# Performance work log

Hardware: AMD Instinct MI355X
Metric: run time of the kernel (lower is better)

## Reference

```python
import jax, jax.numpy as jnp
import numpy as np

N, E, D, G = 20000, 640000, 256, 64
BN_EPS = 1e-5


def setup_inputs() -> dict:
    key = jax.random.key(0)
    ks = jax.random.split(key, 16)
    p = lambda k, sh: jax.random.normal(k, sh, dtype=jnp.float32) * 0.05
    x = jax.random.normal(ks[0], (N, D), dtype=jnp.float32)
    edge_index = jax.random.randint(ks[1], (2, E), 0, N, dtype=jnp.int32)
    batch = jnp.sort(jax.random.randint(ks[2], (N,), 0, G, dtype=jnp.int32))
    return dict(
        x=x, edge_index=edge_index, batch=batch,
        W1=p(ks[3], (D, D)), a1_src=p(ks[4], (D,)), a1_dst=p(ks[5], (D,)), b1=p(ks[6], (D,)),
        W2=p(ks[7], (D, D)), a2_src=p(ks[8], (D,)), a2_dst=p(ks[9], (D,)), b2=p(ks[10], (D,)),
        bn_gamma=jnp.ones((D,), jnp.float32), bn_beta=jnp.zeros((D,), jnp.float32),
        bn_mean=jnp.zeros((D,), jnp.float32), bn_var=jnp.ones((D,), jnp.float32),
        Wl=p(ks[11], (D, D)), bl=p(ks[12], (D,)),
    )


def gat_conv(x, src, dst, W, a_src, a_dst, b):
    # PyG GATConv, heads=1, concat=True, negative_slope=0.2, self-loops already appended
    h = x @ W                               # [N, D]
    alpha_s = h @ a_src                     # [N]
    alpha_d = h @ a_dst                     # [N]
    e = jax.nn.leaky_relu(alpha_s[src] + alpha_d[dst], 0.2)   # [E+N]
    # segment softmax over edges grouped by destination node
    m = jax.ops.segment_max(e, dst, num_segments=N)
    ex = jnp.exp(e - m[dst])
    s = jax.ops.segment_sum(ex, dst, num_segments=N)
    alpha = ex / s[dst]                     # self-loops guarantee s > 0
    out = jax.ops.segment_sum(alpha[:, None] * h[src], dst, num_segments=N)
    return out + b


def reference(x, edge_index, batch, W1, a1_src, a1_dst, b1, W2, a2_src, a2_dst, b2,
              bn_gamma, bn_beta, bn_mean, bn_var, Wl, bl):
    loop = jnp.arange(N, dtype=edge_index.dtype)
    src = jnp.concatenate([edge_index[0], loop])
    dst = jnp.concatenate([edge_index[1], loop])

    h = jax.nn.leaky_relu(gat_conv(x, src, dst, W1, a1_src, a1_dst, b1), 0.01)
    h = jax.nn.leaky_relu(gat_conv(h, src, dst, W2, a2_src, a2_dst, b2), 0.01)
    # BatchNorm over nodes (eval mode, running stats)
    h = (h - bn_mean) * jax.lax.rsqrt(bn_var + BN_EPS) * bn_gamma + bn_beta
    # global mean pool per graph, then linear (dropout is identity in eval)
    sums = jax.ops.segment_sum(h, batch, num_segments=G)           # [G, D]
    cnt = jax.ops.segment_sum(jnp.ones((N,), h.dtype), batch, num_segments=G)
    pooled = sums / jnp.maximum(cnt, 1.0)[:, None]
    return pooled @ Wl.T + bl
```

## Files before the change

### kernel.cpp

```cpp
#include <hip/hip_runtime.h>
#include <hip/hip_bf16.h>

#define NN 20000
#define EE 640000
#define DD 256
#define GG 64
#define ETOT (EE + NN)
#define BN_EPS 1e-5f

typedef short s16x8 __attribute__((ext_vector_type(8)));
typedef short s16x4 __attribute__((ext_vector_type(4)));
typedef float f32x4 __attribute__((ext_vector_type(4)));
typedef int   i32x2 __attribute__((ext_vector_type(2)));

__device__ __forceinline__ unsigned short f2bf_hi(float x) {
    unsigned u = __float_as_uint(x);
    unsigned r = (u + 0x7FFFu + ((u >> 16) & 1u)) >> 16;
    return (unsigned short)r;
}
__device__ __forceinline__ float bf2f(unsigned short h) {
    return __uint_as_float(((unsigned)h) << 16);
}

__global__ void prep_kernel(const int* __restrict__ batch, int* __restrict__ start,
                            float* __restrict__ cntf) {
    int g = threadIdx.x;
    if (g <= GG) {
        if (g == GG) start[GG] = NN;
        else {
            int lo = 0, hi = NN;
            while (lo < hi) { int mid = (lo + hi) >> 1; if (batch[mid] < g) lo = mid + 1; else hi = mid; }
            start[g] = lo;
        }
    }
    __syncthreads();
    if (g < GG) cntf[g] = (float)(start[g + 1] - start[g]);
}

__global__ void hist_kernel(const int* __restrict__ ei, int* __restrict__ counts) {
    int i = blockIdx.x * blockDim.x + threadIdx.x;
    int stride = gridDim.x * blockDim.x;
    for (; i < ETOT; i += stride) {
        int dst = (i < EE) ? ei[EE + i] : (i - EE);
        atomicAdd(&counts[dst], 1);
    }
}

#define SCHUNK 20
__global__ __launch_bounds__(1024) void scan_kernel(const int* __restrict__ counts,
                                                    int* __restrict__ offsets,
                                                    int* __restrict__ cursor) {
    __shared__ int wsums[16];
    int t = threadIdx.x, lane = t & 63, wid = t >> 6;
    int base = t * SCHUNK;
    int loc[SCHUNK];
    int sum = 0;
    #pragma unroll
    for (int i = 0; i < SCHUNK; ++i) {
        int idx = base + i;
        int v = (idx < NN) ? counts[idx] : 0;
        loc[i] = sum; sum += v;
    }
    int x = sum;
    #pragma unroll
    for (int o = 1; o < 64; o <<= 1) { int tv = __shfl_up(x, o, 64); if (lane >= o) x += tv; }
    if (lane == 63) wsums[wid] = x;
    __syncthreads();
    if (wid == 0) {
        int wv = (lane < 16) ? wsums[lane] : 0;
        #pragma unroll
        for (int o = 1; o < 16; o <<= 1) { int tv = __shfl_up(wv, o, 64); if (lane >= o) wv += tv; }
        if (lane < 16) wsums[lane] = wv;
    }
    __syncthreads();
    int tbase = (wid ? wsums[wid - 1] : 0) + x - sum;
    #pragma unroll
    for (int i = 0; i < SCHUNK; ++i) {
        int idx = base + i;
        if (idx < NN) { int e = tbase + loc[i]; offsets[idx] = e; cursor[idx] = e; }
    }
    if (t == 0) offsets[NN] = wsums[15];
}

__global__ void scatter_kernel(const int* __restrict__ ei, int* __restrict__ cursor,
                               int* __restrict__ csr_src) {
    int i = blockIdx.x * blockDim.x + threadIdx.x;
    int stride = gridDim.x * blockDim.x;
    for (; i < ETOT; i += stride) {
        int s, d;
        if (i < EE) { s = ei[i]; d = ei[EE + i]; }
        else        { s = i - EE; d = i - EE; }
        int pos = atomicAdd(&cursor[d], 1);
        csr_src[pos] = s;
    }
}

__global__ __launch_bounds__(256) void convB_kernel(const float* __restrict__ W1,
                                                    const float* __restrict__ W2,
                                                    short* __restrict__ BhT1,
                                                    short* __restrict__ BlT1,
                                                    short* __restrict__ BhT2,
                                                    short* __restrict__ BlT2) {
    int b = blockIdx.x;
    int n = b & 255, which = b >> 8;
    int k = threadIdx.x;
    const float* B = which ? W2 : W1;
    short* Bh = which ? BhT2 : BhT1;
    short* Bl = which ? BlT2 : BlT1;
    float x = B[k * DD + n];
    unsigned short hb = f2bf_hi(x);
    Bh[n * DD + k] = (short)hb;
    Bl[n * DD + k] = (short)f2bf_hi(x - bf2f(hb));
}

#define GBM 128
#define GBN 128
#define GBK 64

__global__ __launch_bounds__(256) void gemm_mfma_kernel(const float* __restrict__ A,
                                                        const short* __restrict__ BhT,
                                                        const short* __restrict__ BlT,
                                                        const float* __restrict__ a_src,
                                                        const float* __restrict__ a_dst,
                                                        short* __restrict__ hb,
                                                        float* __restrict__ asp,
                                                        float* __restrict__ adp,
                                                        int M) {
    __shared__ short As_h[GBM * GBK];
    __shared__ short As_l[GBM * GBK];
    __shared__ short Bs_h[GBN * GBK];
    __shared__ short Bs_l[GBN * GBK];
    int tid = threadIdx.x;
    int row0 = blockIdx.y * GBM;
    int col0 = blockIdx.x * GBN;
    int w = tid >> 6, lane = tid & 63;
    int wr = w >> 1, wc = w & 1;

    f32x4 acc[4][4];
    #pragma unroll
    for (int m = 0; m < 4; ++m)
        #pragma unroll
        for (int n = 0; n < 4; ++n)
            acc[m][n] = (f32x4){0.f, 0.f, 0.f, 0.f};

    int srow = tid >> 3;
    int sslot = tid & 7;

    for (int k0 = 0; k0 < DD; k0 += GBK) {
        __syncthreads();
        #pragma unroll
        for (int p = 0; p < 4; ++p) {
            int r = p * 32 + srow;
            int gr = row0 + r;
            float xv[8];
            if (gr < M) {
                const float4* ap = (const float4*)(A + (size_t)gr * DD + k0 + sslot * 8);
                float4 a0 = ap[0], a1 = ap[1];
                xv[0] = a0.x; xv[1] = a0.y; xv[2] = a0.z; xv[3] = a0.w;
                xv[4] = a1.x; xv[5] = a1.y; xv[6] = a1.z; xv[7] = a1.w;
            } else {
                #pragma unroll
                for (int i = 0; i < 8; ++i) xv[i] = 0.f;
            }
            s16x8 hv, lv;
            #pragma unroll
            for (int i = 0; i < 8; ++i) {
                unsigned short hbb = f2bf_hi(xv[i]);
                hv[i] = (short)hbb;
                lv[i] = (short)f2bf_hi(xv[i] - bf2f(hbb));
            }
            int byte = r * 128 + ((sslot ^ (r & 7)) << 4);
            *(s16x8*)((char*)As_h + byte) = hv;
            *(s16x8*)((char*)As_l + byte) = lv;
            const short* bhp = BhT + (size_t)(col0 + r) * DD + k0 + sslot * 8;
            const short* blp = BlT + (size_t)(col0 + r) * DD + k0 + sslot * 8;
            *(s16x8*)((char*)Bs_h + byte) = *(const s16x8*)bhp;
            *(s16x8*)((char*)Bs_l + byte) = *(const s16x8*)blp;
        }
        __syncthreads();

        #pragma unroll
        for (int ks = 0; ks < 2; ++ks) {
            s16x8 ah[4], al[4], bh[4], bl[4];
            int g = ks * 4 + (lane >> 4);
            #pragma unroll
            for (int m = 0; m < 4; ++m) {
                int r = wr * 64 + m * 16 + (lane & 15);
                int byte = r * 128 + ((g ^ (r & 7)) << 4);
                ah[m] = *(const s16x8*)((char*)As_h + byte);
                al[m] = *(const s16x8*)((char*)As_l + byte);
            }
            #pragma unroll
            for (int n = 0; n < 4; ++n) {
                int c = wc * 64 + n * 16 + (lane & 15);
                int byte = c * 128 + ((g ^ (c & 7)) << 4);
                bh[n] = *(const s16x8*)((char*)Bs_h + byte);
                bl[n] = *(const s16x8*)((char*)Bs_l + byte);
            }
            #pragma unroll
            for (int m = 0; m < 4; ++m)
                #pragma unroll
                for (int n = 0; n < 4; ++n) {
                    acc[m][n] = __builtin_amdgcn_mfma_f32_16x16x32_bf16(ah[m], bh[n], acc[m][n], 0, 0, 0);
                    acc[m][n] = __builtin_amdgcn_mfma_f32_16x16x32_bf16(ah[m], bl[n], acc[m][n], 0, 0, 0);
                    acc[m][n] = __builtin_amdgcn_mfma_f32_16x16x32_bf16(al[m], bh[n], acc[m][n], 0, 0, 0);
                }
        }
    }

    float vsrc[4], vdst[4];
    #pragma unroll
    for (int n = 0; n < 4; ++n) {
        int cg = col0 + wc * 64 + n * 16 + (lane & 15);
        vsrc[n] = a_src[cg];
        vdst[n] = a_dst[cg];
    }
    #pragma unroll
    for (int m = 0; m < 4; ++m) {
        #pragma unroll
        for (int j = 0; j < 4; ++j) {
            float ps = 0.f, pd = 0.f;
            #pragma unroll
            for (int n = 0; n < 4; ++n) {
                float c = acc[m][n][j];
                ps += c * vsrc[n];
                pd += c * vdst[n];
            }
            #pragma unroll
            for (int o = 1; o < 16; o <<= 1) {
                ps += __shfl_xor(ps, o, 64);
                pd += __shfl_xor(pd, o, 64);
            }
            if ((lane & 15) == 0) {
                int rg = row0 + wr * 64 + m * 16 + ((lane >> 4) << 2) + j;
                if (rg < M) {
                    asp[(size_t)(blockIdx.x * 2 + wc) * NN + rg] = ps;
                    adp[(size_t)(blockIdx.x * 2 + wc) * NN + rg] = pd;
                }
            }
        }
    }

    #pragma unroll
    for (int m = 0; m < 4; ++m) {
        int rbase = row0 + wr * 64 + m * 16 + ((lane >> 4) << 2);
        #pragma unroll
        for (int n = 0; n < 4; ++n) {
            int cg = col0 + wc * 64 + n * 16 + (lane & 15);
            #pragma unroll
            for (int j = 0; j < 4; ++j) {
                int rg = rbase + j;
                if (rg < M) hb[(size_t)rg * DD + cg] = (short)f2bf_hi(acc[m][n][j]);
            }
        }
    }
}

__global__ void reduce_kernel(const float* __restrict__ asp, const float* __restrict__ adp,
                              float* __restrict__ as_, float* __restrict__ ad_) {
    int i = blockIdx.x * blockDim.x + threadIdx.x;
    if (i < NN) {
        as_[i] = asp[i] + asp[NN + i] + asp[2 * NN + i] + asp[3 * NN + i];
        ad_[i] = adp[i] + adp[NN + i] + adp[2 * NN + i] + adp[3 * NN + i];
    }
}

__global__ __launch_bounds__(256) void alpha_kernel(const int* __restrict__ csr_src,
                                                    const int* __restrict__ offsets,
                                                    const float* __restrict__ as_,
                                                    const float* __restrict__ ad_,
                                                    int2* __restrict__ pairs) {
    int tid = threadIdx.x;
    int w = tid >> 6, lane = tid & 63;
    int node = blockIdx.x * 4 + w;
    int off = offsets[node];
    int deg = offsets[node + 1] - off;
    float adn = ad_[node];

    if (deg <= 64) {
        int si = 0; float e = -INFINITY;
        if (lane < deg) {
            si = csr_src[off + lane];
            float t = as_[si] + adn;
            e = (t > 0.f) ? t : 0.2f * t;
        }
        float m = e;
        #pragma unroll
        for (int o = 32; o > 0; o >>= 1) m = fmaxf(m, __shfl_xor(m, o, 64));
        float ex = (lane < deg) ? expf(e - m) : 0.f;
        float s = ex;
        #pragma unroll
        for (int o = 32; o > 0; o >>= 1) s += __shfl_xor(s, o, 64);
        if (lane < deg) {
            int2 p; p.x = si; p.y = __float_as_int(ex / s);
            pairs[off + lane] = p;
        }
        return;
    }

    float m = -INFINITY, s = 0.f;
    for (int cs = 0; cs < deg; cs += 64) {
        int cl = min(64, deg - cs);
        float e = -INFINITY;
        if (lane < cl) {
            int si = csr_src[off + cs + lane];
            float t = as_[si] + adn;
            e = (t > 0.f) ? t : 0.2f * t;
        }
        float cm = e;
        #pragma unroll
        for (int o = 32; o > 0; o >>= 1) cm = fmaxf(cm, __shfl_xor(cm, o, 64));
        float newm = fmaxf(m, cm);
        float ex = (lane < cl) ? expf(e - newm) : 0.f;
        float csum = ex;
        #pragma unroll
        for (int o = 32; o > 0; o >>= 1) csum += __shfl_xor(csum, o, 64);
        s = s * expf(m - newm) + csum;
        m = newm;
    }
    float inv = 1.f / s;
    for (int cs = 0; cs < deg; cs += 64) {
        int cl = min(64, deg - cs);
        if (lane < cl) {
            int si = csr_src[off + cs + lane];
            float t = as_[si] + adn;
            float e = (t > 0.f) ? t : 0.2f * t;
            int2 p; p.x = si; p.y = __float_as_int(expf(e - m) * inv);
            pairs[off + cs + lane] = p;
        }
    }
}

__global__ __launch_bounds__(256) void aggregate_kernel(const short* __restrict__ hb,
                                                        const int2* __restrict__ pairs,
                                                        const int* __restrict__ offsets,
                                                        const float* __restrict__ bias,
                                                        float* __restrict__ out) {
    int tid = threadIdx.x;
    int w = tid >> 6, lane = tid & 63;
    int b = blockIdx.x;
    int sl = b & 3;
    int node = ((b >> 2) << 2) + w;
    int eg = lane >> 3;
    int fl = lane & 7;
    int f0 = sl * 64 + fl * 8;
    int off = offsets[node];
    int deg = offsets[node + 1] - off;
    const i32x2* pp = (const i32x2*)pairs + off;

    float accA[8], accB[8];
    #pragma unroll
    for (int k = 0; k < 8; ++k) { accA[k] = 0.f; accB[k] = 0.f; }

    int j = 0;
    i32x2 qA, qB;
    if (deg >= 16) { qA = pp[eg]; qB = pp[8 + eg]; }
    for (; j + 32 <= deg; j += 16) {
        i32x2 nA = pp[j + 16 + eg];
        i32x2 nB = pp[j + 24 + eg];
        s16x8 hA = *(const s16x8*)(hb + (size_t)qA.x * DD + f0);
        s16x8 hB = *(const s16x8*)(hb + (size_t)qB.x * DD + f0);
        float aA = __int_as_float(qA.y), aB = __int_as_float(qB.y);
        #pragma unroll
        for (int k = 0; k < 8; ++k) accA[k] += aA * bf2f((unsigned short)hA[k]);
        #pragma unroll
        for (int k = 0; k < 8; ++k) accB[k] += aB * bf2f((unsigned short)hB[k]);
        qA = nA; qB = nB;
    }
    if (j + 16 <= deg) {
        s16x8 hA = *(const s16x8*)(hb + (size_t)qA.x * DD + f0);
        s16x8 hB = *(const s16x8*)(hb + (size_t)qB.x * DD + f0);
        float aA = __int_as_float(qA.y), aB = __int_as_float(qB.y);
        #pragma unroll
        for (int k = 0; k < 8; ++k) accA[k] += aA * bf2f((unsigned short)hA[k]);
        #pragma unroll
        for (int k = 0; k < 8; ++k) accB[k] += aB * bf2f((unsigned short)hB[k]);
        j += 16;
    }
    {
        if (j + eg < deg) {
            i32x2 p = pp[j + eg];
            s16x8 hv = *(const s16x8*)(hb + (size_t)p.x * DD + f0);
            float a = __int_as_float(p.y);
            #pragma unroll
            for (int k = 0; k < 8; ++k) accA[k] += a * bf2f((unsigned short)hv[k]);
        }
        if (j + 8 + eg < deg) {
            i32x2 p = pp[j + 8 + eg];
            s16x8 hv = *(const s16x8*)(hb + (size_t)p.x * DD + f0);
            float a = __int_as_float(p.y);
            #pragma unroll
            for (int k = 0; k < 8; ++k) accB[k] += a * bf2f((unsigned short)hv[k]);
        }
    }

    f32x4 r0, r1;
    #pragma unroll
    for (int k = 0; k < 8; ++k) {
        float v = accA[k] + accB[k];
        v += __shfl_xor(v, 8, 64);
        v += __shfl_xor(v, 16, 64);
        v += __shfl_xor(v, 32, 64);
        if (k < 4) r0[k] = v; else r1[k - 4] = v;
    }
    if (eg == 0) {
        const f32x4 b0 = *(const f32x4*)(bias + f0);
        const f32x4 b1 = *(const f32x4*)(bias + f0 + 4);
        #pragma unroll
        for (int k = 0; k < 4; ++k) {
            float v0 = r0[k] + b0[k];
            float v1 = r1[k] + b1[k];
            r0[k] = (v0 > 0.f) ? v0 : 0.01f * v0;
            r1[k] = (v1 > 0.f) ? v1 : 0.01f * v1;
        }
        __builtin_nontemporal_store(r0, (f32x4*)(out + (size_t)node * DD + f0));
        __builtin_nontemporal_store(r1, (f32x4*)(out + (size_t)node * DD + f0 + 4));
    }
}

#define PSLICE 8
__global__ __launch_bounds__(256) void pool_kernel(const float* __restrict__ h,
                                                   const int* __restrict__ start,
                                                   float* __restrict__ pool) {
    int g = blockIdx.x >> 3, sl = blockIdx.x & (PSLICE - 1);
    int f = threadIdx.x;
    int s0 = start[g], s1 = start[g + 1];
    float acc = 0.f;
    for (int nd = s0 + sl; nd < s1; nd += PSLICE)
        acc += h[(size_t)nd * DD + f];
    if (acc != 0.f || sl == 0) atomicAdd(&pool[g * DD + f], acc);
}

__global__ __launch_bounds__(256) void final_kernel(const float* __restrict__ pool,
                                                    const float* __restrict__ cnt,
                                                    const float* __restrict__ gam,
                                                    const float* __restrict__ bet,
                                                    const float* __restrict__ mean,
                                                    const float* __restrict__ var,
                                                    const float* __restrict__ Wl,
                                                    const float* __restrict__ bl,
                                                    float* __restrict__ out) {
    __shared__ float p_sh[DD];
    int g = blockIdx.x, j = threadIdx.x;
    float cn = cnt[g];
    float scale = gam[j] * rsqrtf(var[j] + BN_EPS);
    p_sh[j] = (cn > 0.f) ? (pool[g * DD + j] / cn - mean[j]) * scale + bet[j] : 0.f;
    __syncthreads();
    float acc = 0.f;
    for (int fi = 0; fi < DD; ++fi)
        acc += p_sh[fi] * Wl[j * DD + fi];
    out[g * DD + j] = acc + bl[j];
}

extern "C" void kernel_launch(void* const* d_in, const int* in_sizes, int n_in,
                              void* d_out, int out_size, void* d_ws, size_t ws_size,
                              hipStream_t stream) {
    const float* x       = (const float*)d_in[0];
    const int*   ei      = (const int*)d_in[1];
    const int*   batch   = (const int*)d_in[2];
    const float* W1      = (const float*)d_in[3];
    const float* a1_src  = (const float*)d_in[4];
    const float* a1_dst  = (const float*)d_in[5];
    const float* b1      = (const float*)d_in[6];
    const float* W2      = (const float*)d_in[7];
    const float* a2_src  = (const float*)d_in[8];
    const float* a2_dst  = (const float*)d_in[9];
    const float* b2      = (const float*)d_in[10];
    const float* bn_g    = (const float*)d_in[11];
    const float* bn_b    = (const float*)d_in[12];
    const float* bn_m    = (const float*)d_in[13];
    const float* bn_v    = (const float*)d_in[14];
    const float* Wl      = (const float*)d_in[15];
    const float* bl      = (const float*)d_in[16];
    float* out = (float*)d_out;

    char* ws = (char*)d_ws;
    size_t o = 0;
    auto take = [&](size_t bytes) { char* p = ws + o; o += (bytes + 255) & ~(size_t)255; return p; };
    int*   counts  = (int*)  take(NN * 4);
    int*   offsets = (int*)  take((NN + 1) * 4);
    int*   cursor  = (int*)  take(NN * 4);
    int*   csr_src = (int*)  take((size_t)ETOT * 4);
    int2*  pairs   = (int2*) take((size_t)ETOT * 8);
    float* asp     = (float*)take((size_t)4 * NN * 4);
    float* adp     = (float*)take((size_t)4 * NN * 4);
    float* as_     = (float*)take(NN * 4);
    float* ad_     = (float*)take(NN * 4);
    short* hb      = (short*)take((size_t)NN * DD * 2);
    float* bufB    = (float*)take((size_t)NN * DD * 4);
    float* pool    = (float*)take(GG * DD * 4);
    float* cnt     = (float*)take(GG * 4);
    int*   start   = (int*)  take((GG + 1) * 4);
    short* BhT1    = (short*)take((size_t)DD * DD * 2);
    short* BlT1    = (short*)take((size_t)DD * DD * 2);
    short* BhT2    = (short*)take((size_t)DD * DD * 2);
    short* BlT2    = (short*)take((size_t)DD * DD * 2);
    (void)ws_size; (void)in_sizes; (void)n_in; (void)out_size;

    hipMemsetAsync(counts, 0, NN * 4, stream);
    hipMemsetAsync(pool, 0, GG * DD * 4, stream);

    prep_kernel<<<1, 128, 0, stream>>>(batch, start, cnt);
    hist_kernel<<<2579, 256, 0, stream>>>(ei, counts);
    scan_kernel<<<1, 1024, 0, stream>>>(counts, offsets, cursor);
    scatter_kernel<<<2579, 256, 0, stream>>>(ei, cursor, csr_src);

    convB_kernel<<<2 * DD, 256, 0, stream>>>(W1, W2, BhT1, BlT1, BhT2, BlT2);

    dim3 ggrid(DD / GBN, (NN + GBM - 1) / GBM);

    gemm_mfma_kernel<<<ggrid, 256, 0, stream>>>(x, BhT1, BlT1, a1_src, a1_dst, hb, asp, adp, NN);
    reduce_kernel<<<(NN + 255) / 256, 256, 0, stream>>>(asp, adp, as_, ad_);
    alpha_kernel<<<NN / 4, 256, 0, stream>>>(csr_src, offsets, as_, ad_, pairs);
    aggregate_kernel<<<NN, 256, 0, stream>>>(hb, pairs, offsets, b1, bufB);

    gemm_mfma_kernel<<<ggrid, 256, 0, stream>>>(bufB, BhT2, BlT2, a2_src, a2_dst, hb, asp, adp, NN);
    reduce_kernel<<<(NN + 255) / 256, 256, 0, stream>>>(asp, adp, as_, ad_);
    alpha_kernel<<<NN / 4, 256, 0, stream>>>(csr_src, offsets, as_, ad_, pairs);
    aggregate_kernel<<<NN, 256, 0, stream>>>(hb, pairs, offsets, b2, bufB);

    pool_kernel<<<GG * PSLICE, 256, 0, stream>>>(bufB, start, pool);
    final_kernel<<<GG, 256, 0, stream>>>(pool, cnt, bn_g, bn_b, bn_m, bn_v, Wl, bl, out);
}
```

Baseline: 289.2 us.

## Halve GEMM row tile, batch edge loads in CSR build, place self-loops analytically

The GEMM row tile drops from 128 to 64, which doubles the block count over 20000 rows and cuts accumulator registers, in exchange for reloading the B tiles twice as often. The histogram and scatter kernels now each handle four edges per thread with a fixed grid, issuing loads before atomics to improve memory-level parallelism. Self-loops are no longer pushed through the atomics; the scan adds one slot per node and the reduce kernel writes each node's self index into the last slot of its segment. This changes the order of sources within a segment but the sum is unchanged.

After: 271.1 us. -6.3%, faster.

```diff
diff --git a/kernel.cpp b/kernel.cpp
--- a/kernel.cpp
+++ b/kernel.cpp
@@ -9,7 +9,6 @@
 #define BN_EPS 1e-5f
 
 typedef short s16x8 __attribute__((ext_vector_type(8)));
-typedef short s16x4 __attribute__((ext_vector_type(4)));
 typedef float f32x4 __attribute__((ext_vector_type(4)));
 typedef int   i32x2 __attribute__((ext_vector_type(2)));
 
@@ -37,13 +36,20 @@
     if (g < GG) cntf[g] = (float)(start[g + 1] - start[g]);
 }
 
-__global__ void hist_kernel(const int* __restrict__ ei, int* __restrict__ counts) {
-    int i = blockIdx.x * blockDim.x + threadIdx.x;
-    int stride = gridDim.x * blockDim.x;
-    for (; i < ETOT; i += stride) {
-        int dst = (i < EE) ? ei[EE + i] : (i - EE);
-        atomicAdd(&counts[dst], 1);
-    }
+#define HS_BLOCKS 640
+__global__ __launch_bounds__(256) void hist_kernel(const int* __restrict__ ei,
+                                                   int* __restrict__ counts) {
+    int t = blockIdx.x * 256 + threadIdx.x;
+    const int T = HS_BLOCKS * 256;
+    int d[4];
+    #pragma unroll
+    for (int k = 0; k < 4; ++k) {
+        int i = t + k * T;
+        d[k] = (i < EE) ? ei[EE + i] : -1;
+    }
+    #pragma unroll
+    for (int k = 0; k < 4; ++k)
+        if (d[k] >= 0) atomicAdd(&counts[d[k]], 1);
 }
 
 #define SCHUNK 20
@@ -58,7 +64,7 @@
     #pragma unroll
     for (int i = 0; i < SCHUNK; ++i) {
         int idx = base + i;
-        int v = (idx < NN) ? counts[idx] : 0;
+        int v = (idx < NN) ? (counts[idx] + 1) : 0;
         loc[i] = sum; sum += v;
     }
     int x = sum;
@@ -82,17 +88,25 @@
     if (t == 0) offsets[NN] = wsums[15];
 }
 
-__global__ void scatter_kernel(const int* __restrict__ ei, int* __restrict__ cursor,
-                               int* __restrict__ csr_src) {
-    int i = blockIdx.x * blockDim.x + threadIdx.x;
-    int stride = gridDim.x * blockDim.x;
-    for (; i < ETOT; i += stride) {
-        int s, d;
-        if (i < EE) { s = ei[i]; d = ei[EE + i]; }
-        else        { s = i - EE; d = i - EE; }
-        int pos = atomicAdd(&cursor[d], 1);
-        csr_src[pos] = s;
-    }
+__global__ __launch_bounds__(256) void scatter_kernel(const int* __restrict__ ei,
+                                                      int* __restrict__ cursor,
+                                                      int* __restrict__ csr_src) {
+    int t = blockIdx.x * 256 + threadIdx.x;
+    const int T = HS_BLOCKS * 256;
+    int s[4], d[4], pos[4];
+    #pragma unroll
+    for (int k = 0; k < 4; ++k) {
+        int i = t + k * T;
+        bool v = (i < EE);
+        s[k] = v ? ei[i] : 0;
+        d[k] = v ? ei[EE + i] : -1;
+    }
+    #pragma unroll
+    for (int k = 0; k < 4; ++k)
+        if (d[k] >= 0) pos[k] = atomicAdd(&cursor[d[k]], 1);
+    #pragma unroll
+    for (int k = 0; k < 4; ++k)
+        if (d[k] >= 0) csr_src[pos[k]] = s[k];
 }
 
 __global__ __launch_bounds__(256) void convB_kernel(const float* __restrict__ W1,
@@ -113,7 +127,7 @@
     Bl[n * DD + k] = (short)f2bf_hi(x - bf2f(hb));
 }
 
-#define GBM 128
+#define GBM 64
 #define GBN 128
 #define GBK 64
 
@@ -136,9 +150,9 @@
     int w = tid >> 6, lane = tid & 63;
     int wr = w >> 1, wc = w & 1;
 
-    f32x4 acc[4][4];
-    #pragma unroll
-    for (int m = 0; m < 4; ++m)
+    f32x4 acc[2][4];
+    #pragma unroll
+    for (int m = 0; m < 2; ++m)
         #pragma unroll
         for (int n = 0; n < 4; ++n)
             acc[m][n] = (f32x4){0.f, 0.f, 0.f, 0.f};
@@ -149,7 +163,7 @@
     for (int k0 = 0; k0 < DD; k0 += GBK) {
         __syncthreads();
         #pragma unroll
-        for (int p = 0; p < 4; ++p) {
+        for (int p = 0; p < 2; ++p) {
             int r = p * 32 + srow;
             int gr = row0 + r;
             float xv[8];
@@ -172,6 +186,11 @@
             int byte = r * 128 + ((sslot ^ (r & 7)) << 4);
             *(s16x8*)((char*)As_h + byte) = hv;
             *(s16x8*)((char*)As_l + byte) = lv;
+        }
+        #pragma unroll
+        for (int p = 0; p < 4; ++p) {
+            int r = p * 32 + srow;
+            int byte = r * 128 + ((sslot ^ (r & 7)) << 4);
             const short* bhp = BhT + (size_t)(col0 + r) * DD + k0 + sslot * 8;
             const short* blp = BlT + (size_t)(col0 + r) * DD + k0 + sslot * 8;
             *(s16x8*)((char*)Bs_h + byte) = *(const s16x8*)bhp;
@@ -181,11 +200,11 @@
 
         #pragma unroll
         for (int ks = 0; ks < 2; ++ks) {
-            s16x8 ah[4], al[4], bh[4], bl[4];
+            s16x8 ah[2], al[2], bh[4], bl[4];
             int g = ks * 4 + (lane >> 4);
             #pragma unroll
-            for (int m = 0; m < 4; ++m) {
-                int r = wr * 64 + m * 16 + (lane & 15);
+            for (int m = 0; m < 2; ++m) {
+                int r = wr * 32 + m * 16 + (lane & 15);
                 int byte = r * 128 + ((g ^ (r & 7)) << 4);
                 ah[m] = *(const s16x8*)((char*)As_h + byte);
                 al[m] = *(const s16x8*)((char*)As_l + byte);
@@ -198,7 +217,7 @@
                 bl[n] = *(const s16x8*)((char*)Bs_l + byte);
             }
             #pragma unroll
-            for (int m = 0; m < 4; ++m)
+            for (int m = 0; m < 2; ++m)
                 #pragma unroll
                 for (int n = 0; n < 4; ++n) {
                     acc[m][n] = __builtin_amdgcn_mfma_f32_16x16x32_bf16(ah[m], bh[n], acc[m][n], 0, 0, 0);
@@ -216,7 +235,7 @@
         vdst[n] = a_dst[cg];
     }
     #pragma unroll
-    for (int m = 0; m < 4; ++m) {
+    for (int m = 0; m < 2; ++m) {
         #pragma unroll
         for (int j = 0; j < 4; ++j) {
             float ps = 0.f, pd = 0.f;
@@ -232,7 +251,7 @@
                 pd += __shfl_xor(pd, o, 64);
             }
             if ((lane & 15) == 0) {
-                int rg = row0 + wr * 64 + m * 16 + ((lane >> 4) << 2) + j;
+                int rg = row0 + wr * 32 + m * 16 + ((lane >> 4) << 2) + j;
                 if (rg < M) {
                     asp[(size_t)(blockIdx.x * 2 + wc) * NN + rg] = ps;
                     adp[(size_t)(blockIdx.x * 2 + wc) * NN + rg] = pd;
@@ -242,8 +261,8 @@
     }
 
     #pragma unroll
-    for (int m = 0; m < 4; ++m) {
-        int rbase = row0 + wr * 64 + m * 16 + ((lane >> 4) << 2);
+    for (int m = 0; m < 2; ++m) {
+        int rbase = row0 + wr * 32 + m * 16 + ((lane >> 4) << 2);
         #pragma unroll
         for (int n = 0; n < 4; ++n) {
             int cg = col0 + wc * 64 + n * 16 + (lane & 15);
@@ -257,11 +276,14 @@
 }
 
 __global__ void reduce_kernel(const float* __restrict__ asp, const float* __restrict__ adp,
-                              float* __restrict__ as_, float* __restrict__ ad_) {
+                              const int* __restrict__ offsets,
+                              float* __restrict__ as_, float* __restrict__ ad_,
+                              int* __restrict__ csr_src) {
     int i = blockIdx.x * blockDim.x + threadIdx.x;
     if (i < NN) {
         as_[i] = asp[i] + asp[NN + i] + asp[2 * NN + i] + asp[3 * NN + i];
         ad_[i] = adp[i] + adp[NN + i] + adp[2 * NN + i] + adp[3 * NN + i];
+        csr_src[offsets[i + 1] - 1] = i;
     }
 }
 
@@ -501,21 +523,21 @@
     hipMemsetAsync(pool, 0, GG * DD * 4, stream);
 
     prep_kernel<<<1, 128, 0, stream>>>(batch, start, cnt);
-    hist_kernel<<<2579, 256, 0, stream>>>(ei, counts);
+    hist_kernel<<<HS_BLOCKS, 256, 0, stream>>>(ei, counts);
     scan_kernel<<<1, 1024, 0, stream>>>(counts, offsets, cursor);
-    scatter_kernel<<<2579, 256, 0, stream>>>(ei, cursor, csr_src);
+    scatter_kernel<<<HS_BLOCKS, 256, 0, stream>>>(ei, cursor, csr_src);
 
     convB_kernel<<<2 * DD, 256, 0, stream>>>(W1, W2, BhT1, BlT1, BhT2, BlT2);
 
     dim3 ggrid(DD / GBN, (NN + GBM - 1) / GBM);
 
     gemm_mfma_kernel<<<ggrid, 256, 0, stream>>>(x, BhT1, BlT1, a1_src, a1_dst, hb, asp, adp, NN);
-    reduce_kernel<<<(NN + 255) / 256, 256, 0, stream>>>(asp, adp, as_, ad_);
+    reduce_kernel<<<(NN + 255) / 256, 256, 0, stream>>>(asp, adp, offsets, as_, ad_, csr_src);
     alpha_kernel<<<NN / 4, 256, 0, stream>>>(csr_src, offsets, as_, ad_, pairs);
     aggregate_kernel<<<NN, 256, 0, stream>>>(hb, pairs, offsets, b1, bufB);
 
     gemm_mfma_kernel<<<ggrid, 256, 0, stream>>>(bufB, BhT2, BlT2, a2_src, a2_dst, hb, asp, adp, NN);
-    reduce_kernel<<<(NN + 255) / 256, 256, 0, stream>>>(asp, adp, as_, ad_);
+    reduce_kernel<<<(NN + 255) / 256, 256, 0, stream>>>(asp, adp, offsets, as_, ad_, csr_src);
     alpha_kernel<<<NN / 4, 256, 0, stream>>>(csr_src, offsets, as_, ad_, pairs);
     aggregate_kernel<<<NN, 256, 0, stream>>>(hb, pairs, offsets, b2, bufB);
 
```
